# Optimization experiments

Hardware: AMD Instinct MI355X
Metric: run time of the kernel (lower is better)

## Reference

```python
import jax, jax.numpy as jnp
from jax import lax
import numpy as np

T, N, E = 4, 50000, 1600000
IN_CH, HID, OUT = 128, 128, 16


def setup_inputs() -> dict:
    key = jax.random.key(0)
    ks = jax.random.split(key, 10)
    s = lambda fan: 1.0 / np.sqrt(fan)
    return {
        "xs": jax.random.normal(ks[0], (T, N, IN_CH), jnp.float32),
        "edges": jax.random.randint(ks[1], (T, 2, E), 0, N, dtype=jnp.int32),
        "W_gcn": jax.random.normal(ks[2], (HID, IN_CH), jnp.float32) * s(IN_CH),
        "b_gcn": jax.random.normal(ks[3], (HID,), jnp.float32) * s(IN_CH),
        "W_ih": jax.random.normal(ks[4], (3 * HID, HID), jnp.float32) * s(HID),
        "W_hh": jax.random.normal(ks[5], (3 * HID, HID), jnp.float32) * s(HID),
        "b_ih": jax.random.normal(ks[6], (3 * HID,), jnp.float32) * s(HID),
        "b_hh": jax.random.normal(ks[7], (3 * HID,), jnp.float32) * s(HID),
        "W_cls": jax.random.normal(ks[8], (OUT, HID), jnp.float32) * s(HID),
        "b_cls": jax.random.normal(ks[9], (OUT,), jnp.float32) * s(HID),
    }


def reference(xs, edges, W_gcn, b_gcn, W_ih, W_hh, b_ih, b_hh, W_cls, b_cls):
    n = xs.shape[1]
    loop = jnp.arange(n, dtype=edges.dtype)

    def gcn_forward(x, ei):
        src = jnp.concatenate([ei[0], loop])  # add self loops
        dst = jnp.concatenate([ei[1], loop])
        h = x @ W_gcn.T + b_gcn                               # [N, H]
        agg = jax.ops.segment_sum(h[src], dst, num_segments=n)  # scatter_add features
        deg = jax.ops.segment_sum(jnp.ones(dst.shape[0], h.dtype), dst, num_segments=n)
        return jax.nn.relu(agg / jnp.maximum(deg, 1.0)[:, None])

    def gru_cell(z, h):
        gi = z @ W_ih.T + b_ih   # [1, 3H]
        gh = h @ W_hh.T + b_hh
        ir, iz, ig = jnp.split(gi, 3, axis=1)
        hr, hz, hg = jnp.split(gh, 3, axis=1)
        r = jax.nn.sigmoid(ir + hr)
        zg = jax.nn.sigmoid(iz + hz)
        ng = jnp.tanh(ig + r * hg)
        return (1.0 - zg) * ng + zg * h

    def step(h, snap):
        x, ei = snap
        z_mean = gcn_forward(x, ei).mean(axis=0, keepdims=True)  # [1, H]
        return gru_cell(z_mean, h), None

    h0 = jnp.zeros((1, W_hh.shape[1]), xs.dtype)
    h, _ = lax.scan(step, h0, (xs, edges))
    return h @ W_cls.T + b_cls  # [1, OUT]
```

## Files before the change

### kernel.cpp

```cpp
#include <hip/hip_runtime.h>
#include <hip/hip_bf16.h>

typedef unsigned int u32;
typedef unsigned short u16;
typedef unsigned char u8;
typedef __attribute__((ext_vector_type(8))) __bf16 bfrag;
typedef __attribute__((ext_vector_type(4))) float f32x4;
typedef __attribute__((ext_vector_type(2))) float f32x2;

#define T_STEPS 4
#define N_NODES 50000
#define E_EDGES 1600000
#define HID 128
#define OUT_CH 16

#define NCHUNK 128
#define CHUNK (E_EDGES / NCHUNK)
#define NBKT 196
#define BCAP 10240

#define H_STRIDE    6400000u
#define RS_STRIDE   204800u
#define ZP_STRIDE   16384u
#define CSR_STRIDE  3200000u

#define OFF_H     0u
#define OFF_RS    25600000u
#define OFF_ZPAD  26419200u
#define OFF_CSR   26484736u
#define OFF_WB    39284736u
#define OFF_GCNT  39317504u
#define OFF_BBASE 39321600u
#define OFF_RECS  39325696u

__device__ __forceinline__ u8 f32_to_fp8(float v) {
    return (u8)(__builtin_amdgcn_cvt_pk_fp8_f32(v, v, 0, 0) & 0xFF);
}

__global__ void wbf_kernel(const float* __restrict__ W, __bf16* __restrict__ wb) {
    const int i = blockIdx.x * 256 + threadIdx.x;
    wb[i] = (__bf16)W[i];
}

__global__ __launch_bounds__(256) void gemm_mfma_kernel(const float* __restrict__ xs,
                                                        const __bf16* __restrict__ wb,
                                                        const float* __restrict__ b,
                                                        u8* __restrict__ h8_all) {
    const int lane = threadIdx.x & 63;
    const int wv   = threadIdx.x >> 6;
    const int r16  = lane & 15;
    const int quad = lane >> 4;
    const int mb   = blockIdx.x;
    const int t    = blockIdx.y;
    const float* x = xs + (size_t)t * N_NODES * 128;
    u8* h8         = h8_all + (size_t)t * H_STRIDE;

    bfrag Bf[2][4];
#pragma unroll
    for (int nt = 0; nt < 2; ++nt) {
        const int c = wv * 32 + nt * 16 + r16;
#pragma unroll
        for (int ks = 0; ks < 4; ++ks)
            Bf[nt][ks] = *(const bfrag*)(wb + c * 128 + ks * 32 + quad * 8);
    }

    const float* xp = x + (size_t)(mb * 16 + r16) * 128 + quad * 8;
    bfrag Af[4];
#pragma unroll
    for (int ks = 0; ks < 4; ++ks) {
        const float* ap = xp + ks * 32;
#pragma unroll
        for (int j = 0; j < 8; ++j) Af[ks][j] = (__bf16)ap[j];
    }

    f32x4 acc0 = {0.f, 0.f, 0.f, 0.f};
    f32x4 acc1 = {0.f, 0.f, 0.f, 0.f};
#pragma unroll
    for (int ks = 0; ks < 4; ++ks) {
        acc0 = __builtin_amdgcn_mfma_f32_16x16x32_bf16(Af[ks], Bf[0][ks], acc0, 0, 0, 0);
        acc1 = __builtin_amdgcn_mfma_f32_16x16x32_bf16(Af[ks], Bf[1][ks], acc1, 0, 0, 0);
    }

    const int c0 = wv * 32 + r16;
    const float b0 = b[c0], b1 = b[c0 + 16];
#pragma unroll
    for (int r = 0; r < 4; ++r) {
        const size_t row = (size_t)(mb * 16 + quad * 4 + r) * 128;
        h8[row + c0]      = f32_to_fp8(acc0[r] + b0);
        h8[row + c0 + 16] = f32_to_fp8(acc1[r] + b1);
    }
}

__global__ __launch_bounds__(256) void part_kernel(const int* __restrict__ edges,
                                                   u32* __restrict__ gcnt,
                                                   u32* __restrict__ recs) {
    __shared__ u32 bh[NBKT], bc[NBKT];
    const int id  = blockIdx.x;
    const int xcd = id & 7;
    const int t   = xcd >> 1;
    const int c   = ((xcd & 1) << 6) | (id >> 3);
    const int base = c * CHUNK;
    const int* src = edges + (size_t)t * 2 * E_EDGES;
    const int* dst = src + E_EDGES;
    u32* rt = recs + (size_t)t * NBKT * BCAP;
    const int tid = threadIdx.x;

    if (tid < NBKT) bh[tid] = 0;
    __syncthreads();
    for (int i = tid; i < CHUNK; i += 256)
        atomicAdd(&bh[dst[base + i] >> 8], 1u);
    __syncthreads();
    if (tid < NBKT) bc[tid] = atomicAdd(&gcnt[t * 256 + tid], bh[tid]);
    __syncthreads();
    for (int i = tid; i < CHUNK; i += 256) {
        const int d = dst[base + i];
        const int s = src[base + i];
        const int bkt = d >> 8;
        const u32 idx = atomicAdd(&bc[bkt], 1u);
        if (idx < (u32)BCAP)
            rt[(size_t)bkt * BCAP + idx] = ((u32)(d & 255) << 16) | (u32)s;
    }
}

__global__ __launch_bounds__(256) void bscan_kernel(const u32* __restrict__ gcnt,
                                                    u32* __restrict__ bbase) {
    __shared__ u32 sc[256];
    const int tid = threadIdx.x;
    for (int t = 0; t < T_STEPS; ++t) {
        u32 v = (tid < NBKT) ? min(gcnt[t * 256 + tid], (u32)BCAP) : 0u;
        const u32 mine = v;
        sc[tid] = v;
        __syncthreads();
        for (int d = 1; d < 256; d <<= 1) {
            const u32 u = (tid >= d) ? sc[tid - d] : 0u;
            __syncthreads();
            sc[tid] += u;
            __syncthreads();
        }
        if (tid < NBKT) bbase[t * 256 + tid] = sc[tid] - mine;
        __syncthreads();
    }
}

__global__ __launch_bounds__(256) void build_kernel(const u32* __restrict__ recs,
                                                    const u32* __restrict__ gcnt,
                                                    const u32* __restrict__ bbase,
                                                    int* __restrict__ rs_all,
                                                    u16* __restrict__ csr_all) {
    __shared__ u32 ncnt[256];
    __shared__ u32 ncur[256];
    __shared__ u16 cl[BCAP];
    const int id  = blockIdx.x;
    const int xcd = id & 7;
    const int t   = xcd >> 1;
    const int b   = ((xcd & 1) ? 98 : 0) + (id >> 3);
    const int tid = threadIdx.x;
    const u32 cnt   = min(gcnt[t * 256 + b], (u32)BCAP);
    const u32 rbase = bbase[t * 256 + b];
    const u32* rp = recs + ((size_t)t * NBKT + b) * BCAP;
    int* rs  = rs_all + (size_t)t * (RS_STRIDE / 4);
    u16* csr = csr_all + (size_t)t * (CSR_STRIDE / 2);

    ncnt[tid] = 0;
    __syncthreads();
    for (u32 i = tid; i < cnt; i += 256)
        atomicAdd(&ncnt[rp[i] >> 16], 1u);
    __syncthreads();
    const u32 mine = ncnt[tid];
    for (int d = 1; d < 256; d <<= 1) {
        const u32 v = (tid >= d) ? ncnt[tid - d] : 0u;
        __syncthreads();
        ncnt[tid] += v;
        __syncthreads();
    }
    const u32 off = ncnt[tid] - mine;
    ncur[tid] = off;
    const int n = b * 256 + tid;
    if (n <= N_NODES) rs[n] = (int)(rbase + off);
    __syncthreads();
    for (u32 i = tid; i < cnt; i += 256) {
        const u32 r = rp[i];
        const u32 p = atomicAdd(&ncur[r >> 16], 1u);
        cl[p] = (u16)(r & 0xFFFFu);
    }
    __syncthreads();
    for (u32 i = tid; i < cnt; i += 256)
        csr[rbase + i] = cl[i];
}

__global__ __launch_bounds__(256) void gather_kernel(const u32* __restrict__ h8_all,
                                                     const int* __restrict__ rs_all,
                                                     const u16* __restrict__ csr_all,
                                                     float* __restrict__ zp_all) {
    const int lane = threadIdx.x & 63;
    const int wv   = __builtin_amdgcn_readfirstlane((int)(threadIdx.x >> 6));
    const int qh   = lane & 15;
    const int quar = lane >> 4;
    const int id   = blockIdx.x;
    const int xcd  = id & 7;
    const int t    = xcd >> 1;
    const int half = xcd & 1;
    const int kb   = id >> 3;
    const u32* h8d = h8_all + (size_t)t * (H_STRIDE / 4) + half * 16;
    const int* row_start = rs_all + (size_t)t * (RS_STRIDE / 4);
    const u16* csr = csr_all + (size_t)t * (CSR_STRIDE / 2);
    float* z_pad = zp_all + (size_t)t * (ZP_STRIDE / 4);
    const int gw   = kb * 4 + wv;
    const int nw   = 1024 * 4;

    float z0 = 0.f, z1 = 0.f, z2 = 0.f, z3 = 0.f;
    for (int n = gw; n < N_NODES; n += nw) {
        const int rs  = row_start[n];
        const int cnt = row_start[n + 1] - rs;
        const u32 us = h8d[n * 32 + qh];
        const f32x2 slo = __builtin_amdgcn_cvt_pk_f32_fp8(us, 0);
        const f32x2 shi = __builtin_amdgcn_cvt_pk_f32_fp8(us, 1);
        const bool q0 = (quar == 0);
        float a0 = q0 ? slo.x : 0.f;
        float a1 = q0 ? slo.y : 0.f;
        float a2 = q0 ? shi.x : 0.f;
        float a3 = q0 ? shi.y : 0.f;

        const u16* lst = csr + rs;
        int i = 0;
        for (; i + 16 <= cnt; i += 16) {
            const int s0 = lst[i + 0  + quar];
            const int s1 = lst[i + 4  + quar];
            const int s2 = lst[i + 8  + quar];
            const int s3 = lst[i + 12 + quar];
            const u32 u0 = h8d[s0 * 32 + qh];
            const u32 u1 = h8d[s1 * 32 + qh];
            const u32 u2 = h8d[s2 * 32 + qh];
            const u32 u3 = h8d[s3 * 32 + qh];
            const f32x2 l0 = __builtin_amdgcn_cvt_pk_f32_fp8(u0, 0);
            const f32x2 g0 = __builtin_amdgcn_cvt_pk_f32_fp8(u0, 1);
            const f32x2 l1 = __builtin_amdgcn_cvt_pk_f32_fp8(u1, 0);
            const f32x2 g1 = __builtin_amdgcn_cvt_pk_f32_fp8(u1, 1);
            const f32x2 l2 = __builtin_amdgcn_cvt_pk_f32_fp8(u2, 0);
            const f32x2 g2 = __builtin_amdgcn_cvt_pk_f32_fp8(u2, 1);
            const f32x2 l3 = __builtin_amdgcn_cvt_pk_f32_fp8(u3, 0);
            const f32x2 g3 = __builtin_amdgcn_cvt_pk_f32_fp8(u3, 1);
            a0 += (l0.x + l1.x) + (l2.x + l3.x);
            a1 += (l0.y + l1.y) + (l2.y + l3.y);
            a2 += (g0.x + g1.x) + (g2.x + g3.x);
            a3 += (g0.y + g1.y) + (g2.y + g3.y);
        }
        for (; i + 4 <= cnt; i += 4) {
            const int s = lst[i + quar];
            const u32 u = h8d[s * 32 + qh];
            const f32x2 lo = __builtin_amdgcn_cvt_pk_f32_fp8(u, 0);
            const f32x2 hi = __builtin_amdgcn_cvt_pk_f32_fp8(u, 1);
            a0 += lo.x; a1 += lo.y; a2 += hi.x; a3 += hi.y;
        }
        if (quar < cnt - i) {
            const int s = lst[i + quar];
            const u32 u = h8d[s * 32 + qh];
            const f32x2 lo = __builtin_amdgcn_cvt_pk_f32_fp8(u, 0);
            const f32x2 hi = __builtin_amdgcn_cvt_pk_f32_fp8(u, 1);
            a0 += lo.x; a1 += lo.y; a2 += hi.x; a3 += hi.y;
        }
        a0 += __shfl_xor(a0, 16); a0 += __shfl_xor(a0, 32);
        a1 += __shfl_xor(a1, 16); a1 += __shfl_xor(a1, 32);
        a2 += __shfl_xor(a2, 16); a2 += __shfl_xor(a2, 32);
        a3 += __shfl_xor(a3, 16); a3 += __shfl_xor(a3, 32);
        const float inv = 1.0f / (float)(cnt + 1);
        z0 += fmaxf(a0 * inv, 0.f);
        z1 += fmaxf(a1 * inv, 0.f);
        z2 += fmaxf(a2 * inv, 0.f);
        z3 += fmaxf(a3 * inv, 0.f);
    }

    __shared__ float red[4][16][4];
    if (lane < 16) {
        red[wv][lane][0] = z0;
        red[wv][lane][1] = z1;
        red[wv][lane][2] = z2;
        red[wv][lane][3] = z3;
    }
    __syncthreads();
    if (threadIdx.x < 64) {
        const int c = threadIdx.x;
        const int g = c >> 2, m = c & 3;
        float s = 0.f;
#pragma unroll
        for (int w = 0; w < 4; ++w) s += red[w][g][m];
        atomicAdd(&z_pad[(half * 64 + c) * 32], s);
    }
}

__global__ __launch_bounds__(512) void gru_all_kernel(const float* __restrict__ zp_all,
                                                      const float* __restrict__ W_ih,
                                                      const float* __restrict__ W_hh,
                                                      const float* __restrict__ b_ih,
                                                      const float* __restrict__ b_hh,
                                                      const float* __restrict__ W_cls,
                                                      const float* __restrict__ b_cls,
                                                      float* __restrict__ out) {
    __shared__ float zm[128], hs[128], gi[384], gh[384];
    const int tid = threadIdx.x;
    if (tid < 128) hs[tid] = 0.f;
    for (int t = 0; t < T_STEPS; ++t) {
        if (tid < 128)
            zm[tid] = zp_all[(size_t)t * (ZP_STRIDE / 4) + tid * 32] * (1.0f / (float)N_NODES);
        __syncthreads();
        if (tid < 384) {
            float a = b_ih[tid], g = b_hh[tid];
            const float* wi = W_ih + tid * 128;
            const float* wh = W_hh + tid * 128;
#pragma unroll 8
            for (int k = 0; k < 128; ++k) {
                a = fmaf(zm[k], wi[k], a);
                g = fmaf(hs[k], wh[k], g);
            }
            gi[tid] = a;
            gh[tid] = g;
        }
        __syncthreads();
        if (tid < 128) {
            const float r  = 1.f / (1.f + expf(-(gi[tid] + gh[tid])));
            const float zg = 1.f / (1.f + expf(-(gi[128 + tid] + gh[128 + tid])));
            const float ng = tanhf(gi[256 + tid] + r * gh[256 + tid]);
            hs[tid] = (1.f - zg) * ng + zg * hs[tid];
        }
        __syncthreads();
    }
    if (tid < OUT_CH) {
        float a = b_cls[tid];
        const float* wc = W_cls + tid * 128;
#pragma unroll 8
        for (int k = 0; k < 128; ++k) a = fmaf(hs[k], wc[k], a);
        out[tid] = a;
    }
}

extern "C" void kernel_launch(void* const* d_in, const int* in_sizes, int n_in,
                              void* d_out, int out_size, void* d_ws, size_t ws_size,
                              hipStream_t stream) {
    const float* xs    = (const float*)d_in[0];
    const int*   edges = (const int*)d_in[1];
    const float* W_gcn = (const float*)d_in[2];
    const float* b_gcn = (const float*)d_in[3];
    const float* W_ih  = (const float*)d_in[4];
    const float* W_hh  = (const float*)d_in[5];
    const float* b_ih  = (const float*)d_in[6];
    const float* b_hh  = (const float*)d_in[7];
    const float* W_cls = (const float*)d_in[8];
    const float* b_cls = (const float*)d_in[9];
    float* out = (float*)d_out;

    char* ws = (char*)d_ws;
    u8*    h8        = (u8*)(ws + OFF_H);
    int*   row_start = (int*)(ws + OFF_RS);
    float* z_pad     = (float*)(ws + OFF_ZPAD);
    u16*   csr       = (u16*)(ws + OFF_CSR);
    __bf16* wb       = (__bf16*)(ws + OFF_WB);
    u32*   gcnt      = (u32*)(ws + OFF_GCNT);
    u32*   bbase     = (u32*)(ws + OFF_BBASE);
    u32*   recs      = (u32*)(ws + OFF_RECS);

    hipMemsetAsync(z_pad, 0, 4 * ZP_STRIDE, stream);
    hipMemsetAsync(gcnt, 0, 4096, stream);
    wbf_kernel<<<64, 256, 0, stream>>>(W_gcn, wb);

    gemm_mfma_kernel<<<dim3(3125, T_STEPS), 256, 0, stream>>>(xs, wb, b_gcn, h8);
    part_kernel<<<NCHUNK * T_STEPS, 256, 0, stream>>>(edges, gcnt, recs);
    bscan_kernel<<<1, 256, 0, stream>>>(gcnt, bbase);
    build_kernel<<<98 * 8, 256, 0, stream>>>(recs, gcnt, bbase, row_start, csr);
    gather_kernel<<<2048 * T_STEPS, 256, 0, stream>>>((const u32*)h8, row_start, csr, z_pad);
    gru_all_kernel<<<1, 512, 0, stream>>>(z_pad, W_ih, W_hh, b_ih, b_hh,
                                          W_cls, b_cls, out);
}
```

Before: 612.8 us.

## Split fp8 features into half-planes, fuse bucket scan into build, vectorize loads

The GCN projection output is now stored as two separate 64-column planes, one per half of the feature dimension, so each gather half reads a compact 64-byte row and the footprint touched per XCD shrinks, which should improve cache locality. The standalone single-block bucket scan kernel is removed and every build block recomputes the prefix scan over bucket counts in shared memory, saving a launch and a serialized step at the cost of redundant scan work. The GEMM A-fragment loads switch to float4 vector loads.

```diff
diff --git a/kernel.cpp b/kernel.cpp
--- a/kernel.cpp
+++ b/kernel.cpp
@@ -20,6 +20,7 @@
 #define BCAP 10240
 
 #define H_STRIDE    6400000u
+#define HALF_STRIDE 3200000u
 #define RS_STRIDE   204800u
 #define ZP_STRIDE   16384u
 #define CSR_STRIDE  3200000u
@@ -30,8 +31,7 @@
 #define OFF_CSR   26484736u
 #define OFF_WB    39284736u
 #define OFF_GCNT  39317504u
-#define OFF_BBASE 39321600u
-#define OFF_RECS  39325696u
+#define OFF_RECS  39321600u
 
 __device__ __forceinline__ u8 f32_to_fp8(float v) {
     return (u8)(__builtin_amdgcn_cvt_pk_fp8_f32(v, v, 0, 0) & 0xFF);
@@ -68,9 +68,12 @@
     bfrag Af[4];
 #pragma unroll
     for (int ks = 0; ks < 4; ++ks) {
-        const float* ap = xp + ks * 32;
-#pragma unroll
-        for (int j = 0; j < 8; ++j) Af[ks][j] = (__bf16)ap[j];
+        const float4 v0 = *(const float4*)(xp + ks * 32);
+        const float4 v1 = *(const float4*)(xp + ks * 32 + 4);
+        Af[ks][0] = (__bf16)v0.x; Af[ks][1] = (__bf16)v0.y;
+        Af[ks][2] = (__bf16)v0.z; Af[ks][3] = (__bf16)v0.w;
+        Af[ks][4] = (__bf16)v1.x; Af[ks][5] = (__bf16)v1.y;
+        Af[ks][6] = (__bf16)v1.z; Af[ks][7] = (__bf16)v1.w;
     }
 
     f32x4 acc0 = {0.f, 0.f, 0.f, 0.f};
@@ -81,13 +84,16 @@
         acc1 = __builtin_amdgcn_mfma_f32_16x16x32_bf16(Af[ks], Bf[1][ks], acc1, 0, 0, 0);
     }
 
-    const int c0 = wv * 32 + r16;
+    const int c0   = wv * 32 + r16;
+    const int half = wv >> 1;
+    const int col0 = c0 - half * 64;
+    u8* hb = h8 + half * HALF_STRIDE;
     const float b0 = b[c0], b1 = b[c0 + 16];
 #pragma unroll
     for (int r = 0; r < 4; ++r) {
-        const size_t row = (size_t)(mb * 16 + quad * 4 + r) * 128;
-        h8[row + c0]      = f32_to_fp8(acc0[r] + b0);
-        h8[row + c0 + 16] = f32_to_fp8(acc1[r] + b1);
+        const size_t row = (size_t)(mb * 16 + quad * 4 + r) * 64;
+        hb[row + col0]      = f32_to_fp8(acc0[r] + b0);
+        hb[row + col0 + 16] = f32_to_fp8(acc1[r] + b1);
     }
 }
 
@@ -122,44 +128,33 @@
     }
 }
 
-__global__ __launch_bounds__(256) void bscan_kernel(const u32* __restrict__ gcnt,
-                                                    u32* __restrict__ bbase) {
-    __shared__ u32 sc[256];
-    const int tid = threadIdx.x;
-    for (int t = 0; t < T_STEPS; ++t) {
-        u32 v = (tid < NBKT) ? min(gcnt[t * 256 + tid], (u32)BCAP) : 0u;
-        const u32 mine = v;
-        sc[tid] = v;
-        __syncthreads();
-        for (int d = 1; d < 256; d <<= 1) {
-            const u32 u = (tid >= d) ? sc[tid - d] : 0u;
-            __syncthreads();
-            sc[tid] += u;
-            __syncthreads();
-        }
-        if (tid < NBKT) bbase[t * 256 + tid] = sc[tid] - mine;
-        __syncthreads();
-    }
-}
-
 __global__ __launch_bounds__(256) void build_kernel(const u32* __restrict__ recs,
                                                     const u32* __restrict__ gcnt,
-                                                    const u32* __restrict__ bbase,
                                                     int* __restrict__ rs_all,
                                                     u16* __restrict__ csr_all) {
     __shared__ u32 ncnt[256];
     __shared__ u32 ncur[256];
+    __shared__ u32 sc[256];
     __shared__ u16 cl[BCAP];
     const int id  = blockIdx.x;
     const int xcd = id & 7;
     const int t   = xcd >> 1;
     const int b   = ((xcd & 1) ? 98 : 0) + (id >> 3);
     const int tid = threadIdx.x;
-    const u32 cnt   = min(gcnt[t * 256 + b], (u32)BCAP);
-    const u32 rbase = bbase[t * 256 + b];
+    const u32 cnt = min(gcnt[t * 256 + b], (u32)BCAP);
     const u32* rp = recs + ((size_t)t * NBKT + b) * BCAP;
     int* rs  = rs_all + (size_t)t * (RS_STRIDE / 4);
     u16* csr = csr_all + (size_t)t * (CSR_STRIDE / 2);
+
+    sc[tid] = (tid < NBKT) ? min(gcnt[t * 256 + tid], (u32)BCAP) : 0u;
+    __syncthreads();
+    for (int d = 1; d < 256; d <<= 1) {
+        const u32 v = (tid >= d) ? sc[tid - d] : 0u;
+        __syncthreads();
+        sc[tid] += v;
+        __syncthreads();
+    }
+    const u32 rbase = sc[b] - cnt;
 
     ncnt[tid] = 0;
     __syncthreads();
@@ -201,7 +196,7 @@
     const int t    = xcd >> 1;
     const int half = xcd & 1;
     const int kb   = id >> 3;
-    const u32* h8d = h8_all + (size_t)t * (H_STRIDE / 4) + half * 16;
+    const u32* h8d = h8_all + (size_t)t * (H_STRIDE / 4) + half * (HALF_STRIDE / 4);
     const int* row_start = rs_all + (size_t)t * (RS_STRIDE / 4);
     const u16* csr = csr_all + (size_t)t * (CSR_STRIDE / 2);
     float* z_pad = zp_all + (size_t)t * (ZP_STRIDE / 4);
@@ -212,7 +207,7 @@
     for (int n = gw; n < N_NODES; n += nw) {
         const int rs  = row_start[n];
         const int cnt = row_start[n + 1] - rs;
-        const u32 us = h8d[n * 32 + qh];
+        const u32 us = h8d[n * 16 + qh];
         const f32x2 slo = __builtin_amdgcn_cvt_pk_f32_fp8(us, 0);
         const f32x2 shi = __builtin_amdgcn_cvt_pk_f32_fp8(us, 1);
         const bool q0 = (quar == 0);
@@ -228,10 +223,10 @@
             const int s1 = lst[i + 4  + quar];
             const int s2 = lst[i + 8  + quar];
             const int s3 = lst[i + 12 + quar];
-            const u32 u0 = h8d[s0 * 32 + qh];
-            const u32 u1 = h8d[s1 * 32 + qh];
-            const u32 u2 = h8d[s2 * 32 + qh];
-            const u32 u3 = h8d[s3 * 32 + qh];
+            const u32 u0 = h8d[s0 * 16 + qh];
+            const u32 u1 = h8d[s1 * 16 + qh];
+            const u32 u2 = h8d[s2 * 16 + qh];
+            const u32 u3 = h8d[s3 * 16 + qh];
             const f32x2 l0 = __builtin_amdgcn_cvt_pk_f32_fp8(u0, 0);
             const f32x2 g0 = __builtin_amdgcn_cvt_pk_f32_fp8(u0, 1);
             const f32x2 l1 = __builtin_amdgcn_cvt_pk_f32_fp8(u1, 0);
@@ -247,14 +242,14 @@
         }
         for (; i + 4 <= cnt; i += 4) {
             const int s = lst[i + quar];
-            const u32 u = h8d[s * 32 + qh];
+            const u32 u = h8d[s * 16 + qh];
             const f32x2 lo = __builtin_amdgcn_cvt_pk_f32_fp8(u, 0);
             const f32x2 hi = __builtin_amdgcn_cvt_pk_f32_fp8(u, 1);
             a0 += lo.x; a1 += lo.y; a2 += hi.x; a3 += hi.y;
         }
         if (quar < cnt - i) {
             const int s = lst[i + quar];
-            const u32 u = h8d[s * 32 + qh];
+            const u32 u = h8d[s * 16 + qh];
             const f32x2 lo = __builtin_amdgcn_cvt_pk_f32_fp8(u, 0);
             const f32x2 hi = __builtin_amdgcn_cvt_pk_f32_fp8(u, 1);
             a0 += lo.x; a1 += lo.y; a2 += hi.x; a3 += hi.y;
@@ -355,7 +350,6 @@
     u16*   csr       = (u16*)(ws + OFF_CSR);
     __bf16* wb       = (__bf16*)(ws + OFF_WB);
     u32*   gcnt      = (u32*)(ws + OFF_GCNT);
-    u32*   bbase     = (u32*)(ws + OFF_BBASE);
     u32*   recs      = (u32*)(ws + OFF_RECS);
 
     hipMemsetAsync(z_pad, 0, 4 * ZP_STRIDE, stream);
@@ -364,8 +358,7 @@
 
     gemm_mfma_kernel<<<dim3(3125, T_STEPS), 256, 0, stream>>>(xs, wb, b_gcn, h8);
     part_kernel<<<NCHUNK * T_STEPS, 256, 0, stream>>>(edges, gcnt, recs);
-    bscan_kernel<<<1, 256, 0, stream>>>(gcnt, bbase);
-    build_kernel<<<98 * 8, 256, 0, stream>>>(recs, gcnt, bbase, row_start, csr);
+    build_kernel<<<98 * 8, 256, 0, stream>>>(recs, gcnt, row_start, csr);
     gather_kernel<<<2048 * T_STEPS, 256, 0, stream>>>((const u32*)h8, row_start, csr, z_pad);
     gru_all_kernel<<<1, 512, 0, stream>>>(z_pad, W_ih, W_hh, b_ih, b_hh,
                                           W_cls, b_cls, out);
```

New measurement: 562.3 us. -8.2%, faster.
